# Optimization experiments

Measured on AMD Instinct MI355X. Metric: run time of the kernel, lower is better.

Reference implementation:

```python
import jax, jax.numpy as jnp
import numpy as np

N = 50000
E = 800000
IN_C = 128
HID = 16
HEADS = 8
OUT_C = 16
NEG_SLOPE = 0.2


def setup_inputs() -> dict:
    key = jax.random.key(0)
    ks = jax.random.split(key, 10)
    s = 1.0 / np.sqrt(IN_C)
    s2 = 1.0 / np.sqrt(HID * HEADS)
    return {
        "x": jax.random.normal(ks[0], (N, IN_C), jnp.float32),
        "edge_index": jax.random.randint(ks[1], (2, E), 0, N, jnp.int64),
        "W1": jax.random.normal(ks[2], (IN_C, HEADS * HID), jnp.float32) * s,
        "a_src1": jax.random.normal(ks[3], (HEADS, HID), jnp.float32) * s,
        "a_dst1": jax.random.normal(ks[4], (HEADS, HID), jnp.float32) * s,
        "b1": jnp.zeros((HEADS * HID,), jnp.float32),
        "W2": jax.random.normal(ks[5], (HEADS * HID, OUT_C), jnp.float32) * s2,
        "a_src2": jax.random.normal(ks[6], (1, OUT_C), jnp.float32) * s2,
        "a_dst2": jax.random.normal(ks[7], (1, OUT_C), jnp.float32) * s2,
        "b2": jnp.zeros((OUT_C,), jnp.float32),
    }


def gat_layer(x, src, dst, W, a_src, a_dst):
    # x: [N, F_in]; W: [F_in, H*C]; a_src/a_dst: [H, C]
    H, C = a_src.shape
    h = (x @ W).reshape(N, H, C)                       # [N, H, C]
    al_s = jnp.einsum('nhc,hc->nh', h, a_src)          # [N, H]
    al_d = jnp.einsum('nhc,hc->nh', h, a_dst)
    e = jax.nn.leaky_relu(al_s[src] + al_d[dst], NEG_SLOPE)  # [E', H]
    # scatter-softmax over incoming edges of each target node
    m = jax.ops.segment_max(e, dst, num_segments=N)    # [N, H]
    w = jnp.exp(e - m[dst])                            # [E', H]
    denom = jax.ops.segment_sum(w, dst, num_segments=N)
    alpha = w / denom[dst]                             # [E', H]
    out = jax.ops.segment_sum(h[src] * alpha[:, :, None], dst, num_segments=N)
    return out                                         # [N, H, C]


def reference(x, edge_index, W1, a_src1, a_dst1, b1, W2, a_src2, a_dst2, b2):
    loops = jnp.arange(N, dtype=edge_index.dtype)
    src = jnp.concatenate([edge_index[0], loops])
    dst = jnp.concatenate([edge_index[1], loops])
    # layer 1: heads=8, concat=True
    h1 = gat_layer(x, src, dst, W1, a_src1, a_dst1).reshape(N, -1) + b1
    h1 = jax.nn.elu(h1)
    # layer 2: heads=1, concat=False (single head -> mean is identity)
    h2 = gat_layer(h1, src, dst, W2, a_src2, a_dst2)[:, 0, :] + b2
    return h2
```

## Files before the change

### kernel.cpp

```cpp
#include <hip/hip_runtime.h>
#include <hip/hip_fp16.h>
#include <math.h>

#define N_NODES 50000
#define NE      800000
#define INC     128
#define F1      128
#define HEADS   8
#define HID     16
#define OUTC    16
#define NEG     0.2f
#define NBKT    196
#define NPART   128
#define N1BLK   ((N_NODES + 63) / 64)

union H4 { ushort4 u; __half h[4]; };
union H8 { uint4 u; __half h[8]; };

typedef _Float16 f16x8 __attribute__((ext_vector_type(8)));
typedef float    f32x4 __attribute__((ext_vector_type(4)));

__global__ __launch_bounds__(256) void prep_kernel(const int* __restrict__ ei,
                                                   int* __restrict__ cnt,
                                                   const float* __restrict__ W1,
                                                   const float* __restrict__ as1,
                                                   const float* __restrict__ ad1,
                                                   __half* __restrict__ W1t,
                                                   __half* __restrict__ waT) {
    __shared__ int h[NBKT];
    int b = blockIdx.x, tid = threadIdx.x;
    if (b < NPART) {
        for (int i = tid; i < NBKT; i += 256) h[i] = 0;
        __syncthreads();
        for (int e = b * 256 + tid; e < NE; e += NPART * 256)
            atomicAdd(&h[ei[NE + e] >> 8], 1);
        __syncthreads();
        for (int i = tid; i < NBKT; i += 256) cnt[i * NPART + b] = h[i];
    } else if (b < NPART + 64) {
        int i = (b - NPART) * 256 + tid;
        int k = i >> 7, nn = i & 127;
        W1t[nn * 128 + k] = __float2half(W1[k * 128 + nn]);
    } else {
        int i = (b - NPART - 64) * 256 + tid;
        int col = i & 15, k = i >> 4;
        int hh = col & 7;
        const float* av = (col < 8) ? as1 : ad1;
        float s = 0.f;
        #pragma unroll
        for (int cc = 0; cc < 16; ++cc)
            s += W1[k * 128 + hh * 16 + cc] * av[hh * 16 + cc];
        waT[col * 128 + k] = __float2half(s);
    }
}

__global__ __launch_bounds__(1024) void scan25k(int* __restrict__ cnt) {
    __shared__ int part[1024];
    const int TOT = NBKT * NPART;
    const int PER = (TOT + 1023) / 1024;
    int tid = threadIdx.x;
    int base = tid * PER;
    int s = 0;
    for (int i = 0; i < PER; ++i) {
        int idx = base + i;
        if (idx < TOT) s += cnt[idx];
    }
    part[tid] = s; __syncthreads();
    for (int off = 1; off < 1024; off <<= 1) {
        int t = (tid >= off) ? part[tid - off] : 0;
        __syncthreads();
        part[tid] += t;
        __syncthreads();
    }
    int run = part[tid] - s;
    for (int i = 0; i < PER; ++i) {
        int idx = base + i;
        if (idx < TOT) { int v = cnt[idx]; cnt[idx] = run; run += v; }
    }
}

__global__ __launch_bounds__(256) void scatter_node1_kernel(
    const int* __restrict__ ei, const int* __restrict__ cnt, int* __restrict__ tmp,
    const float* __restrict__ x, const __half* __restrict__ W1t,
    const __half* __restrict__ waT,
    __half* __restrict__ hfeat, float* __restrict__ als, float* __restrict__ ald)
{
    __shared__ _Float16 Xh[64 * 136];
    __shared__ _Float16 Wt[128 * 136];
    int b = blockIdx.x, tid = threadIdx.x;

    if (b < NPART) {
        int* cur = (int*)Xh;
        for (int i = tid; i < NBKT; i += 256) cur[i] = cnt[i * NPART + b];
        __syncthreads();
        for (int e = b * 256 + tid; e < NE; e += NPART * 256) {
            int s = ei[e], d = ei[NE + e];
            int p = atomicAdd(&cur[d >> 8], 1);
            tmp[p] = s | ((d & 255) << 16);
        }
        return;
    }

    int n0 = (b - NPART) * 64;

    for (int idx = tid; idx < 128 * 16; idx += 256) {
        int row = idx >> 4, c8 = (idx & 15) * 8;
        *(uint4*)(&Wt[row * 136 + c8]) = ((const uint4*)W1t)[idx];
    }
    for (int idx = tid; idx < 64 * 32; idx += 256) {
        int m = idx >> 5, f4 = idx & 31;
        int n = n0 + m;
        float4 v = (n < N_NODES) ? ((const float4*)(x + (size_t)n * INC))[f4]
                                 : make_float4(0.f, 0.f, 0.f, 0.f);
        union { unsigned long long u; _Float16 h[4]; } p;
        p.h[0] = (_Float16)v.x; p.h[1] = (_Float16)v.y;
        p.h[2] = (_Float16)v.z; p.h[3] = (_Float16)v.w;
        *(unsigned long long*)(&Xh[m * 136 + f4 * 4]) = p.u;
    }
    __syncthreads();

    int wave = tid >> 6, lane = tid & 63;
    int colL = lane & 15, q = lane >> 4;
    int nb = wave * 32;

    f32x4 acc[4][2];
    #pragma unroll
    for (int mt = 0; mt < 4; ++mt)
        #pragma unroll
        for (int nt = 0; nt < 2; ++nt)
            acc[mt][nt] = (f32x4){0.f, 0.f, 0.f, 0.f};
    f32x4 acc2 = (f32x4){0.f, 0.f, 0.f, 0.f};

    #pragma unroll
    for (int kb = 0; kb < 4; ++kb) {
        int ko = kb * 32 + q * 8;
        f16x8 b0 = *(const f16x8*)(&Wt[(nb +  0 + colL) * 136 + ko]);
        f16x8 b1 = *(const f16x8*)(&Wt[(nb + 16 + colL) * 136 + ko]);
        #pragma unroll
        for (int mt = 0; mt < 4; ++mt) {
            f16x8 a = *(const f16x8*)(&Xh[(mt * 16 + colL) * 136 + ko]);
            acc[mt][0] = __builtin_amdgcn_mfma_f32_16x16x32_f16(a, b0, acc[mt][0], 0, 0, 0);
            acc[mt][1] = __builtin_amdgcn_mfma_f32_16x16x32_f16(a, b1, acc[mt][1], 0, 0, 0);
        }
        f16x8 bw = *(const f16x8*)(waT + colL * 128 + ko);
        f16x8 aw = *(const f16x8*)(&Xh[(wave * 16 + colL) * 136 + ko]);
        acc2 = __builtin_amdgcn_mfma_f32_16x16x32_f16(aw, bw, acc2, 0, 0, 0);
    }

    #pragma unroll
    for (int nt = 0; nt < 2; ++nt) {
        int col = nb + nt * 16 + colL;
        #pragma unroll
        for (int mt = 0; mt < 4; ++mt) {
            f32x4 d = acc[mt][nt];
            #pragma unroll
            for (int r = 0; r < 4; ++r) {
                int node = n0 + mt * 16 + q * 4 + r;
                if (node < N_NODES) hfeat[(size_t)node * F1 + col] = __float2half(d[r]);
            }
        }
    }
    #pragma unroll
    for (int r = 0; r < 4; ++r) {
        int node = n0 + wave * 16 + q * 4 + r;
        if (node < N_NODES) {
            if (colL < 8) als[node * 8 + colL] = acc2[r];
            else          ald[node * 8 + (colL - 8)] = acc2[r];
        }
    }
}

__global__ __launch_bounds__(256) void bucket_sort(const int* __restrict__ tmp,
                                                   const int* __restrict__ cnt,
                                                   int* __restrict__ rowstart,
                                                   int* __restrict__ csr) {
    __shared__ int h[256];
    int b = blockIdx.x, tid = threadIdx.x;
    int base = cnt[b * NPART];
    int end  = (b == NBKT - 1) ? NE : cnt[(b + 1) * NPART];
    h[tid] = 0; __syncthreads();
    for (int i = base + tid; i < end; i += 256)
        atomicAdd(&h[(tmp[i] >> 16) & 255], 1);
    __syncthreads();
    int v = h[tid];
    for (int off = 1; off < 256; off <<= 1) {
        int t = (tid >= off) ? h[tid - off] : 0;
        __syncthreads();
        h[tid] += t;
        __syncthreads();
    }
    int excl = h[tid] - v;
    int n = (b << 8) + tid;
    if (n <= N_NODES) rowstart[n] = base + excl;
    __syncthreads();
    h[tid] = excl;
    __syncthreads();
    for (int i = base + tid; i < end; i += 256) {
        int e = tmp[i];
        int p = base + atomicAdd(&h[(e >> 16) & 255], 1);
        csr[p] = e & 0xFFFF;
    }
}

__global__ __launch_bounds__(256) void agg1_node2_kernel(
    const int* __restrict__ rowstart, const int* __restrict__ csr,
    const __half* __restrict__ h1, const float* __restrict__ als,
    const float* __restrict__ ald, const float* __restrict__ b1,
    const float* __restrict__ W2, const float* __restrict__ a_s2,
    const float* __restrict__ a_d2,
    __half* __restrict__ h2, float* __restrict__ als2, float* __restrict__ ald2)
{
    __shared__ float    W2l[F1 * OUTC];
    __shared__ _Float16 hbuf[16][136];

    int tid = threadIdx.x;
    for (int i = tid; i < F1 * OUTC; i += 256) W2l[i] = W2[i];

    int nl = tid >> 4;
    int n = blockIdx.x * 16 + nl;
    int lane = tid & 15;
    int c = lane * 8;
    int head = lane >> 1;
    float aldn = ald[n * 8 + head];
    float v0 = als[n * 8 + head] + aldn;
    v0 = fmaxf(v0, NEG * v0);
    float w0 = __expf(v0);
    float sum = w0;
    float a[8];
    {
        H8 hs; hs.u = *(const uint4*)(h1 + (size_t)n * F1 + c);
        #pragma unroll
        for (int i = 0; i < 8; ++i) a[i] = w0 * __half2float(hs.h[i]);
    }
    int r0 = rowstart[n], r1 = rowstart[n + 1];

    float vA = 0.f, vB = 0.f;
    H8 hA, hB; hA.u = make_uint4(0,0,0,0); hB.u = hA.u;
    int sC = 0, sD = 0;
    if (r0 < r1) {
        int s = csr[r0];
        float t = als[s * 8 + head] + aldn;
        vA = fmaxf(t, NEG * t);
        hA.u = *(const uint4*)(h1 + (size_t)s * F1 + c);
    }
    if (r0 + 1 < r1) {
        int s = csr[r0 + 1];
        float t = als[s * 8 + head] + aldn;
        vB = fmaxf(t, NEG * t);
        hB.u = *(const uint4*)(h1 + (size_t)s * F1 + c);
    }
    if (r0 + 2 < r1) sC = csr[r0 + 2];
    if (r0 + 3 < r1) sD = csr[r0 + 3];

    int k = r0;
    for (; k + 1 < r1; k += 2) {
        float vcA = vA, vcB = vB;
        H8 hcA = hA, hcB = hB;
        int sE = (k + 4 < r1) ? csr[k + 4] : 0;
        int sF = (k + 5 < r1) ? csr[k + 5] : 0;
        if (k + 2 < r1) {
            float t = als[sC * 8 + head] + aldn;
            vA = fmaxf(t, NEG * t);
            hA.u = *(const uint4*)(h1 + (size_t)sC * F1 + c);
        }
        if (k + 3 < r1) {
            float t = als[sD * 8 + head] + aldn;
            vB = fmaxf(t, NEG * t);
            hB.u = *(const uint4*)(h1 + (size_t)sD * F1 + c);
        }
        sC = sE; sD = sF;
        float wA = __expf(vcA), wB = __expf(vcB);
        sum += wA + wB;
        #pragma unroll
        for (int i = 0; i < 8; ++i) {
            a[i] = fmaf(wA, __half2float(hcA.h[i]), a[i]);
            a[i] = fmaf(wB, __half2float(hcB.h[i]), a[i]);
        }
    }
    if (k < r1) {
        float wA = __expf(vA);
        sum += wA;
        #pragma unroll
        for (int i = 0; i < 8; ++i) a[i] = fmaf(wA, __half2float(hA.h[i]), a[i]);
    }

    float inv = 1.0f / sum;
    f16x8 hv;
    #pragma unroll
    for (int i = 0; i < 8; ++i) {
        float o = a[i] * inv + b1[c + i];
        o = o > 0.f ? o : (__expf(o) - 1.0f);
        hv[i] = (_Float16)o;
    }
    *(f16x8*)(&hbuf[nl][c]) = hv;
    __syncthreads();

    int c2 = tid & 15;
    float acc = 0.f;
    #pragma unroll
    for (int k8 = 0; k8 < 16; ++k8) {
        f16x8 xv = *(const f16x8*)(&hbuf[nl][k8 * 8]);
        #pragma unroll
        for (int j = 0; j < 8; ++j)
            acc = fmaf((float)xv[j], W2l[(k8 * 8 + j) * OUTC + c2], acc);
    }
    h2[(size_t)n * OUTC + c2] = __float2half(acc);

    float ps = acc * a_s2[c2];
    float pd = acc * a_d2[c2];
    #pragma unroll
    for (int m = 1; m < 16; m <<= 1) {
        ps += __shfl_xor(ps, m, 64);
        pd += __shfl_xor(pd, m, 64);
    }
    if (c2 == 0) { als2[n] = ps; ald2[n] = pd; }
}

__global__ __launch_bounds__(256) void agg2_kernel(
    const int* __restrict__ rowstart, const int* __restrict__ csr,
    const __half* __restrict__ h2, const float* __restrict__ als,
    const float* __restrict__ ald, const float* __restrict__ b2,
    float* __restrict__ out)
{
    int tid = threadIdx.x;
    int n = blockIdx.x * 64 + (tid >> 2);
    if (n >= N_NODES) return;
    int c = (tid & 3) * 4;
    float aldn = ald[n];
    float v0 = als[n] + aldn;
    v0 = fmaxf(v0, NEG * v0);
    float w0 = __expf(v0);
    float sum = w0;
    H4 hs; hs.u = *(const ushort4*)(h2 + (size_t)n * OUTC + c);
    float a0 = w0 * __half2float(hs.h[0]), a1 = w0 * __half2float(hs.h[1]);
    float a2 = w0 * __half2float(hs.h[2]), a3 = w0 * __half2float(hs.h[3]);
    int r0 = rowstart[n], r1 = rowstart[n + 1];

    float vA = 0.f, vB = 0.f;
    H4 hA, hB; hA.u = make_ushort4(0,0,0,0); hB.u = hA.u;
    int sC = 0, sD = 0;
    if (r0 < r1) {
        int s = csr[r0];
        float t = als[s] + aldn;
        vA = fmaxf(t, NEG * t);
        hA.u = *(const ushort4*)(h2 + (size_t)s * OUTC + c);
    }
    if (r0 + 1 < r1) {
        int s = csr[r0 + 1];
        float t = als[s] + aldn;
        vB = fmaxf(t, NEG * t);
        hB.u = *(const ushort4*)(h2 + (size_t)s * OUTC + c);
    }
    if (r0 + 2 < r1) sC = csr[r0 + 2];
    if (r0 + 3 < r1) sD = csr[r0 + 3];

    int k = r0;
    for (; k + 1 < r1; k += 2) {
        float vcA = vA, vcB = vB;
        H4 hcA = hA, hcB = hB;
        int sE = (k + 4 < r1) ? csr[k + 4] : 0;
        int sF = (k + 5 < r1) ? csr[k + 5] : 0;
        if (k + 2 < r1) {
            float t = als[sC] + aldn;
            vA = fmaxf(t, NEG * t);
            hA.u = *(const ushort4*)(h2 + (size_t)sC * OUTC + c);
        }
        if (k + 3 < r1) {
            float t = als[sD] + aldn;
            vB = fmaxf(t, NEG * t);
            hB.u = *(const ushort4*)(h2 + (size_t)sD * OUTC + c);
        }
        sC = sE; sD = sF;
        float wA = __expf(vcA), wB = __expf(vcB);
        sum += wA + wB;
        a0 = fmaf(wA, __half2float(hcA.h[0]), a0); a0 = fmaf(wB, __half2float(hcB.h[0]), a0);
        a1 = fmaf(wA, __half2float(hcA.h[1]), a1); a1 = fmaf(wB, __half2float(hcB.h[1]), a1);
        a2 = fmaf(wA, __half2float(hcA.h[2]), a2); a2 = fmaf(wB, __half2float(hcB.h[2]), a2);
        a3 = fmaf(wA, __half2float(hcA.h[3]), a3); a3 = fmaf(wB, __half2float(hcB.h[3]), a3);
    }
    if (k < r1) {
        float wA = __expf(vA);
        sum += wA;
        a0 = fmaf(wA, __half2float(hA.h[0]), a0);
        a1 = fmaf(wA, __half2float(hA.h[1]), a1);
        a2 = fmaf(wA, __half2float(hA.h[2]), a2);
        a3 = fmaf(wA, __half2float(hA.h[3]), a3);
    }

    float inv = 1.0f / sum;
    float4 bv = *(const float4*)(b2 + c);
    float4 o;
    o.x = a0 * inv + bv.x; o.y = a1 * inv + bv.y;
    o.z = a2 * inv + bv.z; o.w = a3 * inv + bv.w;
    *(float4*)(out + (size_t)n * OUTC + c) = o;
}

extern "C" void kernel_launch(void* const* d_in, const int* in_sizes, int n_in,
                              void* d_out, int out_size, void* d_ws, size_t ws_size,
                              hipStream_t stream)
{
    const float* x   = (const float*)d_in[0];
    const int*   ei  = (const int*)  d_in[1];
    const float* W1  = (const float*)d_in[2];
    const float* as1 = (const float*)d_in[3];
    const float* ad1 = (const float*)d_in[4];
    const float* b1  = (const float*)d_in[5];
    const float* W2  = (const float*)d_in[6];
    const float* as2 = (const float*)d_in[7];
    const float* ad2 = (const float*)d_in[8];
    const float* b2  = (const float*)d_in[9];
    float* out = (float*)d_out;

    char* wsb = (char*)d_ws;
    const size_t SZ_H1 = (size_t)N_NODES * F1 * sizeof(__half);
    __half* h1h = (__half*)wsb;
    __half* h1b = (__half*)(wsb + SZ_H1);
    float*  als1 = (float*)(wsb + 2 * SZ_H1);
    float*  ald1 = als1 + (size_t)N_NODES * 8;
    __half* h2f  = (__half*)(ald1 + (size_t)N_NODES * 8);
    float*  als2 = (float*)(h2f + (size_t)N_NODES * OUTC);
    float*  ald2 = als2 + N_NODES;
    __half* w1t  = (__half*)(ald2 + N_NODES);
    __half* waT  = w1t + INC * F1;
    int*    tmp  = (int*)(waT + 16 * INC);
    int*    cnt  = tmp + NE;
    int*    csr  = cnt + NBKT * NPART;
    int*    rowstart = csr + NE;
    (void)h1b;

    prep_kernel <<<NPART + 72, 256, 0, stream>>>(ei, cnt, W1, as1, ad1, w1t, waT);
    scan25k     <<<1, 1024, 0, stream>>>(cnt);
    scatter_node1_kernel<<<NPART + N1BLK, 256, 0, stream>>>(ei, cnt, tmp,
                                                            x, w1t, waT, h1h, als1, ald1);
    bucket_sort <<<NBKT, 256, 0, stream>>>(tmp, cnt, rowstart, csr);

    agg1_node2_kernel<<<N_NODES / 16, 256, 0, stream>>>(rowstart, csr, h1h, als1, ald1, b1,
                                                        W2, as2, ad2, h2f, als2, ald2);

    agg2_kernel<<<(N_NODES + 63) / 64, 256, 0, stream>>>(rowstart, csr, h2f, als2, ald2, b2, out);
}
```

Baseline: 213.9 us.

## Build CSR with global per-node atomics and unroll layer-1 aggregation by four

Replaces the two-level bucket sort (partitioned bucket histograms, scan, bucketed scatter, per-bucket local sort) with a direct CSR build: a zeroing kernel, per-destination global atomic degree counts, a single-block scan producing rowstart and cursor arrays, and an atomic scatter of sources straight into csr. This drops the bucket_sort kernel launch and the tmp pass, at the cost of many contended global atomics and a non-deterministic edge order within each row. Separately, the layer-1 aggregation loop is software-pipelined four edges deep instead of two, which raises memory-level parallelism at the cost of more registers.

```diff
diff --git a/kernel.cpp b/kernel.cpp
--- a/kernel.cpp
+++ b/kernel.cpp
@@ -10,7 +10,6 @@
 #define HID     16
 #define OUTC    16
 #define NEG     0.2f
-#define NBKT    196
 #define NPART   128
 #define N1BLK   ((N_NODES + 63) / 64)
 
@@ -20,22 +19,22 @@
 typedef _Float16 f16x8 __attribute__((ext_vector_type(8)));
 typedef float    f32x4 __attribute__((ext_vector_type(4)));
 
+__global__ __launch_bounds__(256) void zero_deg(int* __restrict__ deg) {
+    int i = blockIdx.x * 256 + threadIdx.x;
+    if (i <= N_NODES) deg[i] = 0;
+}
+
 __global__ __launch_bounds__(256) void prep_kernel(const int* __restrict__ ei,
-                                                   int* __restrict__ cnt,
+                                                   int* __restrict__ deg,
                                                    const float* __restrict__ W1,
                                                    const float* __restrict__ as1,
                                                    const float* __restrict__ ad1,
                                                    __half* __restrict__ W1t,
                                                    __half* __restrict__ waT) {
-    __shared__ int h[NBKT];
     int b = blockIdx.x, tid = threadIdx.x;
     if (b < NPART) {
-        for (int i = tid; i < NBKT; i += 256) h[i] = 0;
-        __syncthreads();
         for (int e = b * 256 + tid; e < NE; e += NPART * 256)
-            atomicAdd(&h[ei[NE + e] >> 8], 1);
-        __syncthreads();
-        for (int i = tid; i < NBKT; i += 256) cnt[i * NPART + b] = h[i];
+            atomicAdd(&deg[ei[NE + e]], 1);
     } else if (b < NPART + 64) {
         int i = (b - NPART) * 256 + tid;
         int k = i >> 7, nn = i & 127;
@@ -53,16 +52,17 @@
     }
 }
 
-__global__ __launch_bounds__(1024) void scan25k(int* __restrict__ cnt) {
+__global__ __launch_bounds__(1024) void scan50k(const int* __restrict__ deg,
+                                                int* __restrict__ rowstart,
+                                                int* __restrict__ pos) {
     __shared__ int part[1024];
-    const int TOT = NBKT * NPART;
-    const int PER = (TOT + 1023) / 1024;
+    const int PER = (N_NODES + 1023) / 1024;
     int tid = threadIdx.x;
     int base = tid * PER;
     int s = 0;
     for (int i = 0; i < PER; ++i) {
         int idx = base + i;
-        if (idx < TOT) s += cnt[idx];
+        if (idx < N_NODES) s += deg[idx];
     }
     part[tid] = s; __syncthreads();
     for (int off = 1; off < 1024; off <<= 1) {
@@ -74,12 +74,13 @@
     int run = part[tid] - s;
     for (int i = 0; i < PER; ++i) {
         int idx = base + i;
-        if (idx < TOT) { int v = cnt[idx]; cnt[idx] = run; run += v; }
-    }
+        if (idx < N_NODES) { rowstart[idx] = run; pos[idx] = run; run += deg[idx]; }
+    }
+    if (tid == 0) rowstart[N_NODES] = NE;
 }
 
 __global__ __launch_bounds__(256) void scatter_node1_kernel(
-    const int* __restrict__ ei, const int* __restrict__ cnt, int* __restrict__ tmp,
+    const int* __restrict__ ei, int* __restrict__ pos, int* __restrict__ csr,
     const float* __restrict__ x, const __half* __restrict__ W1t,
     const __half* __restrict__ waT,
     __half* __restrict__ hfeat, float* __restrict__ als, float* __restrict__ ald)
@@ -89,13 +90,10 @@
     int b = blockIdx.x, tid = threadIdx.x;
 
     if (b < NPART) {
-        int* cur = (int*)Xh;
-        for (int i = tid; i < NBKT; i += 256) cur[i] = cnt[i * NPART + b];
-        __syncthreads();
         for (int e = b * 256 + tid; e < NE; e += NPART * 256) {
             int s = ei[e], d = ei[NE + e];
-            int p = atomicAdd(&cur[d >> 8], 1);
-            tmp[p] = s | ((d & 255) << 16);
+            int p = atomicAdd(&pos[d], 1);
+            csr[p] = s;
         }
         return;
     }
@@ -166,38 +164,6 @@
             if (colL < 8) als[node * 8 + colL] = acc2[r];
             else          ald[node * 8 + (colL - 8)] = acc2[r];
         }
-    }
-}
-
-__global__ __launch_bounds__(256) void bucket_sort(const int* __restrict__ tmp,
-                                                   const int* __restrict__ cnt,
-                                                   int* __restrict__ rowstart,
-                                                   int* __restrict__ csr) {
-    __shared__ int h[256];
-    int b = blockIdx.x, tid = threadIdx.x;
-    int base = cnt[b * NPART];
-    int end  = (b == NBKT - 1) ? NE : cnt[(b + 1) * NPART];
-    h[tid] = 0; __syncthreads();
-    for (int i = base + tid; i < end; i += 256)
-        atomicAdd(&h[(tmp[i] >> 16) & 255], 1);
-    __syncthreads();
-    int v = h[tid];
-    for (int off = 1; off < 256; off <<= 1) {
-        int t = (tid >= off) ? h[tid - off] : 0;
-        __syncthreads();
-        h[tid] += t;
-        __syncthreads();
-    }
-    int excl = h[tid] - v;
-    int n = (b << 8) + tid;
-    if (n <= N_NODES) rowstart[n] = base + excl;
-    __syncthreads();
-    h[tid] = excl;
-    __syncthreads();
-    for (int i = base + tid; i < end; i += 256) {
-        int e = tmp[i];
-        int p = base + atomicAdd(&h[(e >> 16) & 255], 1);
-        csr[p] = e & 0xFFFF;
     }
 }
 
@@ -232,55 +198,60 @@
         for (int i = 0; i < 8; ++i) a[i] = w0 * __half2float(hs.h[i]);
     }
     int r0 = rowstart[n], r1 = rowstart[n + 1];
-
-    float vA = 0.f, vB = 0.f;
-    H8 hA, hB; hA.u = make_uint4(0,0,0,0); hB.u = hA.u;
-    int sC = 0, sD = 0;
-    if (r0 < r1) {
-        int s = csr[r0];
-        float t = als[s * 8 + head] + aldn;
-        vA = fmaxf(t, NEG * t);
-        hA.u = *(const uint4*)(h1 + (size_t)s * F1 + c);
-    }
-    if (r0 + 1 < r1) {
-        int s = csr[r0 + 1];
-        float t = als[s * 8 + head] + aldn;
-        vB = fmaxf(t, NEG * t);
-        hB.u = *(const uint4*)(h1 + (size_t)s * F1 + c);
-    }
-    if (r0 + 2 < r1) sC = csr[r0 + 2];
-    if (r0 + 3 < r1) sD = csr[r0 + 3];
-
     int k = r0;
-    for (; k + 1 < r1; k += 2) {
-        float vcA = vA, vcB = vB;
-        H8 hcA = hA, hcB = hB;
-        int sE = (k + 4 < r1) ? csr[k + 4] : 0;
-        int sF = (k + 5 < r1) ? csr[k + 5] : 0;
-        if (k + 2 < r1) {
-            float t = als[sC * 8 + head] + aldn;
-            vA = fmaxf(t, NEG * t);
-            hA.u = *(const uint4*)(h1 + (size_t)sC * F1 + c);
-        }
-        if (k + 3 < r1) {
-            float t = als[sD * 8 + head] + aldn;
-            vB = fmaxf(t, NEG * t);
-            hB.u = *(const uint4*)(h1 + (size_t)sD * F1 + c);
-        }
-        sC = sE; sD = sF;
-        float wA = __expf(vcA), wB = __expf(vcB);
-        sum += wA + wB;
+
+    float vA = 0.f, vB = 0.f, vC = 0.f, vD = 0.f;
+    H8 hA, hB, hC, hD;
+    hA.u = make_uint4(0,0,0,0); hB.u = hA.u; hC.u = hA.u; hD.u = hA.u;
+    int sE = 0, sF = 0, sG = 0, sH = 0;
+
+    if (k     < r1) { int s = csr[k];     float t = als[s*8+head]+aldn; vA = fmaxf(t, NEG*t); hA.u = *(const uint4*)(h1+(size_t)s*F1+c); }
+    if (k + 1 < r1) { int s = csr[k + 1]; float t = als[s*8+head]+aldn; vB = fmaxf(t, NEG*t); hB.u = *(const uint4*)(h1+(size_t)s*F1+c); }
+    if (k + 2 < r1) { int s = csr[k + 2]; float t = als[s*8+head]+aldn; vC = fmaxf(t, NEG*t); hC.u = *(const uint4*)(h1+(size_t)s*F1+c); }
+    if (k + 3 < r1) { int s = csr[k + 3]; float t = als[s*8+head]+aldn; vD = fmaxf(t, NEG*t); hD.u = *(const uint4*)(h1+(size_t)s*F1+c); }
+    if (k + 4 < r1) sE = csr[k + 4];
+    if (k + 5 < r1) sF = csr[k + 5];
+    if (k + 6 < r1) sG = csr[k + 6];
+    if (k + 7 < r1) sH = csr[k + 7];
+
+    for (; k + 3 < r1; k += 4) {
+        float vcA = vA, vcB = vB, vcC = vC, vcD = vD;
+        H8 hcA = hA, hcB = hB, hcC = hC, hcD = hD;
+        int sI = (k + 8  < r1) ? csr[k + 8]  : 0;
+        int sJ = (k + 9  < r1) ? csr[k + 9]  : 0;
+        int sK = (k + 10 < r1) ? csr[k + 10] : 0;
+        int sL = (k + 11 < r1) ? csr[k + 11] : 0;
+        if (k + 4 < r1) { float t = als[sE*8+head]+aldn; vA = fmaxf(t, NEG*t); hA.u = *(const uint4*)(h1+(size_t)sE*F1+c); }
+        if (k + 5 < r1) { float t = als[sF*8+head]+aldn; vB = fmaxf(t, NEG*t); hB.u = *(const uint4*)(h1+(size_t)sF*F1+c); }
+        if (k + 6 < r1) { float t = als[sG*8+head]+aldn; vC = fmaxf(t, NEG*t); hC.u = *(const uint4*)(h1+(size_t)sG*F1+c); }
+        if (k + 7 < r1) { float t = als[sH*8+head]+aldn; vD = fmaxf(t, NEG*t); hD.u = *(const uint4*)(h1+(size_t)sH*F1+c); }
+        sE = sI; sF = sJ; sG = sK; sH = sL;
+        float wA = __expf(vcA), wB = __expf(vcB), wC = __expf(vcC), wD = __expf(vcD);
+        sum += (wA + wB) + (wC + wD);
         #pragma unroll
         for (int i = 0; i < 8; ++i) {
-            a[i] = fmaf(wA, __half2float(hcA.h[i]), a[i]);
-            a[i] = fmaf(wB, __half2float(hcB.h[i]), a[i]);
+            float ai = a[i];
+            ai = fmaf(wA, __half2float(hcA.h[i]), ai);
+            ai = fmaf(wB, __half2float(hcB.h[i]), ai);
+            ai = fmaf(wC, __half2float(hcC.h[i]), ai);
+            ai = fmaf(wD, __half2float(hcD.h[i]), ai);
+            a[i] = ai;
         }
     }
     if (k < r1) {
-        float wA = __expf(vA);
-        sum += wA;
-        #pragma unroll
-        for (int i = 0; i < 8; ++i) a[i] = fmaf(wA, __half2float(hA.h[i]), a[i]);
+        float w = __expf(vA); sum += w;
+        #pragma unroll
+        for (int i = 0; i < 8; ++i) a[i] = fmaf(w, __half2float(hA.h[i]), a[i]);
+    }
+    if (k + 1 < r1) {
+        float w = __expf(vB); sum += w;
+        #pragma unroll
+        for (int i = 0; i < 8; ++i) a[i] = fmaf(w, __half2float(hB.h[i]), a[i]);
+    }
+    if (k + 2 < r1) {
+        float w = __expf(vC); sum += w;
+        #pragma unroll
+        for (int i = 0; i < 8; ++i) a[i] = fmaf(w, __half2float(hC.h[i]), a[i]);
     }
 
     float inv = 1.0f / sum;
@@ -412,26 +383,24 @@
 
     char* wsb = (char*)d_ws;
     const size_t SZ_H1 = (size_t)N_NODES * F1 * sizeof(__half);
-    __half* h1h = (__half*)wsb;
-    __half* h1b = (__half*)(wsb + SZ_H1);
-    float*  als1 = (float*)(wsb + 2 * SZ_H1);
+    __half* h1h  = (__half*)wsb;
+    float*  als1 = (float*)(wsb + SZ_H1);
     float*  ald1 = als1 + (size_t)N_NODES * 8;
     __half* h2f  = (__half*)(ald1 + (size_t)N_NODES * 8);
     float*  als2 = (float*)(h2f + (size_t)N_NODES * OUTC);
     float*  ald2 = als2 + N_NODES;
     __half* w1t  = (__half*)(ald2 + N_NODES);
     __half* waT  = w1t + INC * F1;
-    int*    tmp  = (int*)(waT + 16 * INC);
-    int*    cnt  = tmp + NE;
-    int*    csr  = cnt + NBKT * NPART;
+    int*    deg  = (int*)(waT + 16 * INC);
+    int*    pos  = deg + (N_NODES + 1);
+    int*    csr  = pos + N_NODES;
     int*    rowstart = csr + NE;
-    (void)h1b;
-
-    prep_kernel <<<NPART + 72, 256, 0, stream>>>(ei, cnt, W1, as1, ad1, w1t, waT);
-    scan25k     <<<1, 1024, 0, stream>>>(cnt);
-    scatter_node1_kernel<<<NPART + N1BLK, 256, 0, stream>>>(ei, cnt, tmp,
+
+    zero_deg    <<<(N_NODES + 256) / 256, 256, 0, stream>>>(deg);
+    prep_kernel <<<NPART + 72, 256, 0, stream>>>(ei, deg, W1, as1, ad1, w1t, waT);
+    scan50k     <<<1, 1024, 0, stream>>>(deg, rowstart, pos);
+    scatter_node1_kernel<<<NPART + N1BLK, 256, 0, stream>>>(ei, pos, csr,
                                                             x, w1t, waT, h1h, als1, ald1);
-    bucket_sort <<<NBKT, 256, 0, stream>>>(tmp, cnt, rowstart, csr);
 
     agg1_node2_kernel<<<N_NODES / 16, 256, 0, stream>>>(rowstart, csr, h1h, als1, ald1, b1,
                                                         W2, as2, ad2, h2f, als2, ald2);
```

Measured after the change: 352.6 us. 1.65x slower.
